# Performance work log

Hardware: AMD Instinct MI355X
Metric: run time of the kernel (lower is better)

The kernel has to match this reference:

```python
import jax, jax.numpy as jnp
import numpy as np

N_CLASS = 8192
FEAT_DIM = 1024
BATCH = 1024
PROTO_M = 0.95
TEMP = 0.1
BASE_TEMP = 0.1
EPS = 1e-12  # F.normalize eps


def setup_inputs() -> dict:
    key = jax.random.key(0)
    k1, k2, k3 = jax.random.split(key, 3)
    features = jax.random.normal(k1, (BATCH, FEAT_DIM), dtype=jnp.float32)
    labels = jax.random.randint(k2, (BATCH,), 0, N_CLASS)
    prototypes = jax.random.normal(k3, (N_CLASS, FEAT_DIM), dtype=jnp.float32)
    # init_class_prototypes ends with F.normalize(prototypes, dim=1)
    prototypes = prototypes / jnp.maximum(
        jnp.linalg.norm(prototypes, axis=1, keepdims=True), EPS)
    return {"features": features, "labels": labels, "prototypes": prototypes}


def _ema_update(prototypes, features, labels):
    # Sequential per-sample EMA scatter update (order matters for repeated labels),
    # expressed as a lax.scan over the batch.
    def step(protos, fl):
        f, l = fl
        row = protos[l] * PROTO_M + f * (1.0 - PROTO_M)
        row = row / jnp.maximum(jnp.linalg.norm(row), EPS)  # F.normalize(dim=0)
        return protos.at[l].set(row), None

    protos, _ = jax.lax.scan(step, prototypes, (features, labels))
    return protos


def reference(features, labels, prototypes):
    protos = _ema_update(prototypes, features, labels)  # [C, D]
    logits = jnp.matmul(protos, protos.T) / TEMP        # [C, C]
    exp_l = jnp.exp(logits)
    # mask = off-diagonal ones (labels are arange(n_class)), so the masked sum
    # is the row sum minus the diagonal; mask.sum(1) == n_class - 1 (never NaN).
    sum_neg = exp_l.sum(axis=1) - jnp.diagonal(exp_l)   # [C]
    mean_prob_neg = jnp.log(sum_neg / jnp.float32(N_CLASS - 1))
    loss = (TEMP / BASE_TEMP) * jnp.mean(mean_prob_neg)
    return loss
```

## Files before the change

kernel.cpp:

```cpp
#include <hip/hip_runtime.h>
#include <math.h>

#define C 8192
#define D 1024
#define BATCH 1024
#define PM 0.95f
#define PMC 0.05f
#define INVT_SCALED 0.15625f

typedef unsigned char u8;
typedef __attribute__((ext_vector_type(16))) float f32x16;

#define GLOBAL_AS(p) ((const __attribute__((address_space(1))) void*)(p))
#define LDS_AS(p) ((__attribute__((address_space(3))) void*)(p))

__global__ __launch_bounds__(256) void ema_split_kernel(const float* __restrict__ feat,
                                                        const int* __restrict__ labels,
                                                        const float* __restrict__ protos,
                                                        u8* __restrict__ P8,
                                                        float* __restrict__ rowsum,
                                                        float* __restrict__ out) {
    __shared__ int sl[BATCH];
    const int t = threadIdx.x, w = t >> 6, lane = t & 63;
    const int c = blockIdx.x * 4 + w;

    if (blockIdx.x < 32) rowsum[blockIdx.x * 256 + t] = 0.0f;
    if (blockIdx.x == 0 && t == 0) out[0] = 0.0f;

    for (int i = t; i < BATCH; i += 256) sl[i] = labels[i];
    __syncthreads();

    float4 v[4];
    #pragma unroll
    for (int s = 0; s < 4; ++s)
        v[s] = *(const float4*)(protos + (size_t)c * D + s * 256 + lane * 4);

    for (int base = 0; base < BATCH; base += 64) {
        unsigned long long mask = __ballot(sl[base + lane] == c);
        while (mask) {
            const int b = __ffsll((long long)mask) - 1;
            mask &= mask - 1;
            const int idx = base + b;
            float ss = 0.0f;
            #pragma unroll
            for (int s = 0; s < 4; ++s) {
                const float4 f = *(const float4*)(feat + (size_t)idx * D + s * 256 + lane * 4);
                v[s].x = v[s].x * PM + f.x * PMC;
                v[s].y = v[s].y * PM + f.y * PMC;
                v[s].z = v[s].z * PM + f.z * PMC;
                v[s].w = v[s].w * PM + f.w * PMC;
                ss += v[s].x * v[s].x + v[s].y * v[s].y + v[s].z * v[s].z + v[s].w * v[s].w;
            }
            #pragma unroll
            for (int off = 32; off > 0; off >>= 1) ss += __shfl_xor(ss, off);
            const float inv = 1.0f / fmaxf(sqrtf(ss), 1e-12f);
            #pragma unroll
            for (int s = 0; s < 4; ++s) {
                v[s].x *= inv; v[s].y *= inv; v[s].z *= inv; v[s].w *= inv;
            }
        }
    }

    u8* ob = P8 + (size_t)(c >> 5) * 32768 + (c & 31) * 8;
    #pragma unroll
    for (int s = 0; s < 4; ++s) {
        const int k0 = s * 256 + lane * 4;
        const size_t off = (size_t)(k0 >> 4) * 512 + ((k0 >> 3) & 1) * 256 + (k0 & 7);
        int p = __builtin_amdgcn_cvt_pk_fp8_f32(v[s].x * 8.0f, v[s].y * 8.0f, 0, false);
        p = __builtin_amdgcn_cvt_pk_fp8_f32(v[s].z * 8.0f, v[s].w * 8.0f, p, true);
        *(unsigned int*)(ob + off) = (unsigned int)p;
    }
}

__global__ __launch_bounds__(256, 4) void gram8_kernel(const u8* __restrict__ P8,
                                                       float* __restrict__ rowsum) {
    __shared__ u8 lds[5][8192];
    const int t = threadIdx.x, w = t >> 6, lane = t & 63;
    const int bb = blockIdx.x;

    const int qi = w >> 1, qj = w & 1;
    const int aoff = qi * 2048 + lane * 8;
    const int boff = 4096 + qj * 2048 + lane * 8;
    const int ldsA = w * 1024, ldsB = 4096 + w * 1024;

    const int nt = (bb % 33 == 0) ? 3 : 2;

    f32x16 acc[2][2];
    long fa[2][2], fb[2][2];

#define STAGE(KC, BUF)                                                         \
    __builtin_amdgcn_global_load_lds(GLOBAL_AS(gsrcA + (size_t)(KC) * 1024),   \
                                     LDS_AS(&lds[BUF][ldsA]), 16, 0, 0);       \
    __builtin_amdgcn_global_load_lds(GLOBAL_AS(gsrcB + (size_t)(KC) * 1024),   \
                                     LDS_AS(&lds[BUF][ldsB]), 16, 0, 0);

#define PF(SET, BUF, KK)                                                       \
    fa[SET][0] = *(const long*)&lds[BUF][aoff + (KK) * 512];                   \
    fa[SET][1] = *(const long*)&lds[BUF][aoff + 1024 + (KK) * 512];            \
    fb[SET][0] = *(const long*)&lds[BUF][boff + (KK) * 512];                   \
    fb[SET][1] = *(const long*)&lds[BUF][boff + 1024 + (KK) * 512];

#define MFMA4(SET)                                                             \
    acc[0][0] = __builtin_amdgcn_mfma_f32_32x32x16_fp8_fp8(fa[SET][0], fb[SET][0], acc[0][0], 0, 0, 0); \
    acc[0][1] = __builtin_amdgcn_mfma_f32_32x32x16_fp8_fp8(fa[SET][0], fb[SET][1], acc[0][1], 0, 0, 0); \
    acc[1][0] = __builtin_amdgcn_mfma_f32_32x32x16_fp8_fp8(fa[SET][1], fb[SET][0], acc[1][0], 0, 0, 0); \
    acc[1][1] = __builtin_amdgcn_mfma_f32_32x32x16_fp8_fp8(fa[SET][1], fb[SET][1], acc[1][1], 0, 0, 0);

#define WAITV(N) asm volatile("s_waitcnt vmcnt(" #N ")" ::: "memory")

    for (int tt = 0; tt < nt; ++tt) {
        const int l = (tt == 2) ? 2048 + bb / 33 : 2 * bb + tt;
        int rem = l, bi = 0;
        while (rem >= 64 - bi) { rem -= 64 - bi; ++bi; }
        const int bj = bi + rem;
        const bool diag = (bi == bj);

        const u8* gsrcA = P8 + (size_t)(bi * 4 + w) * 32768 + lane * 16;
        const u8* gsrcB = P8 + (size_t)(bj * 4 + w) * 32768 + lane * 16;

        #pragma unroll
        for (int a = 0; a < 2; ++a)
            #pragma unroll
            for (int b = 0; b < 2; ++b)
                #pragma unroll
                for (int e = 0; e < 16; ++e) acc[a][b][e] = 0.0f;

        __syncthreads();

        STAGE(0, 0); STAGE(1, 1); STAGE(2, 2); STAGE(3, 3);
        WAITV(4);
        __builtin_amdgcn_s_barrier();
        PF(0, 0, 0);

        int cb = 0;
        for (int kc = 0; kc < 28; ++kc) {
            const int sb = (cb >= 1) ? cb - 1 : 4;
            STAGE(kc + 4, sb);
            const int nb = (cb == 4) ? 0 : cb + 1;
            PF(1, cb, 1);
            MFMA4(0);
            PF(0, nb, 0);
            MFMA4(1);
            WAITV(4);
            __builtin_amdgcn_s_barrier();
            cb = nb;
        }
        PF(1, 3, 1); MFMA4(0);
        PF(0, 4, 0); MFMA4(1);
        WAITV(2); __builtin_amdgcn_s_barrier();
        PF(1, 4, 1); MFMA4(0);
        PF(0, 0, 0); MFMA4(1);
        WAITV(0); __builtin_amdgcn_s_barrier();
        PF(1, 0, 1); MFMA4(0);
        PF(0, 1, 0); MFMA4(1);
        PF(1, 1, 1); MFMA4(0);
        MFMA4(1);

        __syncthreads();
        float* rpart = (float*)&lds[0][0];
        float* cpart = (float*)&lds[0][512];
        if (t < 128) { rpart[t] = 0.0f; cpart[t] = 0.0f; }
        __syncthreads();
        const int half = lane >> 5, col = lane & 31;
        float csum[2] = {0.0f, 0.0f};
        #pragma unroll
        for (int ti = 0; ti < 2; ++ti) {
            float rs[16];
            #pragma unroll
            for (int reg = 0; reg < 16; ++reg) rs[reg] = 0.0f;
            #pragma unroll
            for (int tj = 0; tj < 2; ++tj) {
                const int lj = qj * 64 + tj * 32 + col;
                #pragma unroll
                for (int reg = 0; reg < 16; ++reg) {
                    const int li = qi * 64 + ti * 32 + (reg & 3) + 8 * (reg >> 2) + 4 * half;
                    float e = __expf(acc[ti][tj][reg] * INVT_SCALED);
                    if (diag && li >= lj) e = 0.0f;
                    rs[reg] += e;
                    csum[tj] += e;
                }
            }
            #pragma unroll
            for (int reg = 0; reg < 16; ++reg) {
                float v = rs[reg];
                v += __shfl_xor(v, 1); v += __shfl_xor(v, 2); v += __shfl_xor(v, 4);
                v += __shfl_xor(v, 8); v += __shfl_xor(v, 16);
                if (col == 0)
                    atomicAdd(&rpart[qi * 64 + ti * 32 + (reg & 3) + 8 * (reg >> 2) + 4 * half], v);
            }
        }
        #pragma unroll
        for (int tj = 0; tj < 2; ++tj) {
            float v = csum[tj];
            v += __shfl_xor(v, 32);
            if (half == 0) atomicAdd(&cpart[qj * 64 + tj * 32 + col], v);
        }
        __syncthreads();
        if (t < 128) atomicAdd(&rowsum[bi * 128 + t], rpart[t]);
        else         atomicAdd(&rowsum[bj * 128 + (t - 128)], cpart[t - 128]);
    }
}

__global__ __launch_bounds__(256) void final2_kernel(const float* __restrict__ rowsum,
                                                     float* __restrict__ out) {
    __shared__ float red[4];
    const int t = threadIdx.x;
    const int i = blockIdx.x * 256 + t;
    float v = logf(rowsum[i] * (1.0f / (float)(C - 1)));
    #pragma unroll
    for (int off = 32; off > 0; off >>= 1) v += __shfl_down(v, off);
    if ((t & 63) == 0) red[t >> 6] = v;
    __syncthreads();
    if (t == 0)
        atomicAdd(out, (red[0] + red[1] + red[2] + red[3]) * (1.0f / (float)C));
}

extern "C" void kernel_launch(void* const* d_in, const int* in_sizes, int n_in,
                              void* d_out, int out_size, void* d_ws, size_t ws_size,
                              hipStream_t stream) {
    const float* feat = (const float*)d_in[0];
    const int* labels = (const int*)d_in[1];
    const float* protos = (const float*)d_in[2];
    float* out = (float*)d_out;
    float* rowsum = (float*)d_ws;
    u8* P8 = (u8*)((char*)d_ws + 32768);

    ema_split_kernel<<<C / 4, 256, 0, stream>>>(feat, labels, protos, P8, rowsum, out);
    gram8_kernel<<<1024, 256, 0, stream>>>(P8, rowsum);
    final2_kernel<<<C / 256, 256, 0, stream>>>(rowsum, out);
}
```

Measured before the change: 159.8 us.

## Give each wave private LDS double buffer and drop per-step block barriers in gram kernel

Each wave now stages its own A and B row slices into a private double-buffered LDS region, so the 5-deep shared ring and its per-iteration block barriers are replaced by per-wave vmcnt/lgkmcnt waits. The tile-to-block mapping is changed to a strided strip assignment (r = bb&7) that interleaves short and long triangle strips, likely for L2 locality and load balance. The cost is that waves no longer share staged data, so each wave loads twice as much from global/L2 and the prefetch depth drops from four stages to two. That raises memory traffic and latency exposure in exchange for removing barrier stalls.

```diff
diff --git a/kernel.cpp b/kernel.cpp
--- a/kernel.cpp
+++ b/kernel.cpp
@@ -74,49 +74,60 @@
 
 __global__ __launch_bounds__(256, 4) void gram8_kernel(const u8* __restrict__ P8,
                                                        float* __restrict__ rowsum) {
-    __shared__ u8 lds[5][8192];
+    __shared__ u8 lds[4][2][4096];
     const int t = threadIdx.x, w = t >> 6, lane = t & 63;
     const int bb = blockIdx.x;
+    const int r = bb & 7;
+    const int s = bb >> 3;
 
     const int qi = w >> 1, qj = w & 1;
-    const int aoff = qi * 2048 + lane * 8;
-    const int boff = 4096 + qj * 2048 + lane * 8;
-    const int ldsA = w * 1024, ldsB = 4096 + w * 1024;
-
-    const int nt = (bb % 33 == 0) ? 3 : 2;
+
+    int nt = 2, extra = 0;
+    if (s == 0 || s == 33 || s == 66 || s == 99) { nt = 3; extra = 256 + s / 33; }
 
     f32x16 acc[2][2];
     long fa[2][2], fb[2][2];
 
-#define STAGE(KC, BUF)                                                         \
-    __builtin_amdgcn_global_load_lds(GLOBAL_AS(gsrcA + (size_t)(KC) * 1024),   \
-                                     LDS_AS(&lds[BUF][ldsA]), 16, 0, 0);       \
-    __builtin_amdgcn_global_load_lds(GLOBAL_AS(gsrcB + (size_t)(KC) * 1024),   \
-                                     LDS_AS(&lds[BUF][ldsB]), 16, 0, 0);
-
-#define PF(SET, BUF, KK)                                                       \
-    fa[SET][0] = *(const long*)&lds[BUF][aoff + (KK) * 512];                   \
-    fa[SET][1] = *(const long*)&lds[BUF][aoff + 1024 + (KK) * 512];            \
-    fb[SET][0] = *(const long*)&lds[BUF][boff + (KK) * 512];                   \
-    fb[SET][1] = *(const long*)&lds[BUF][boff + 1024 + (KK) * 512];
-
-#define MFMA4(SET)                                                             \
-    acc[0][0] = __builtin_amdgcn_mfma_f32_32x32x16_fp8_fp8(fa[SET][0], fb[SET][0], acc[0][0], 0, 0, 0); \
-    acc[0][1] = __builtin_amdgcn_mfma_f32_32x32x16_fp8_fp8(fa[SET][0], fb[SET][1], acc[0][1], 0, 0, 0); \
-    acc[1][0] = __builtin_amdgcn_mfma_f32_32x32x16_fp8_fp8(fa[SET][1], fb[SET][0], acc[1][0], 0, 0, 0); \
-    acc[1][1] = __builtin_amdgcn_mfma_f32_32x32x16_fp8_fp8(fa[SET][1], fb[SET][1], acc[1][1], 0, 0, 0);
+#define STAGE(KC, BUF)                                                             \
+    __builtin_amdgcn_global_load_lds(GLOBAL_AS(gA + (size_t)(KC) * 1024),          \
+                                     LDS_AS(&lds[w][BUF][0]), 16, 0, 0);           \
+    __builtin_amdgcn_global_load_lds(GLOBAL_AS(gA + (size_t)(KC) * 1024 + 32768),  \
+                                     LDS_AS(&lds[w][BUF][1024]), 16, 0, 0);        \
+    __builtin_amdgcn_global_load_lds(GLOBAL_AS(gB + (size_t)(KC) * 1024),          \
+                                     LDS_AS(&lds[w][BUF][2048]), 16, 0, 0);        \
+    __builtin_amdgcn_global_load_lds(GLOBAL_AS(gB + (size_t)(KC) * 1024 + 32768),  \
+                                     LDS_AS(&lds[w][BUF][3072]), 16, 0, 0);
+
+#define PF(KK, BUF)                                                                \
+    fa[KK][0] = *(const long*)&lds[w][BUF][(KK) * 512 + lane * 8];                 \
+    fa[KK][1] = *(const long*)&lds[w][BUF][1024 + (KK) * 512 + lane * 8];          \
+    fb[KK][0] = *(const long*)&lds[w][BUF][2048 + (KK) * 512 + lane * 8];          \
+    fb[KK][1] = *(const long*)&lds[w][BUF][3072 + (KK) * 512 + lane * 8];
+
+#define MFMA4(KK)                                                                  \
+    acc[0][0] = __builtin_amdgcn_mfma_f32_32x32x16_fp8_fp8(fa[KK][0], fb[KK][0], acc[0][0], 0, 0, 0); \
+    acc[0][1] = __builtin_amdgcn_mfma_f32_32x32x16_fp8_fp8(fa[KK][0], fb[KK][1], acc[0][1], 0, 0, 0); \
+    acc[1][0] = __builtin_amdgcn_mfma_f32_32x32x16_fp8_fp8(fa[KK][1], fb[KK][0], acc[1][0], 0, 0, 0); \
+    acc[1][1] = __builtin_amdgcn_mfma_f32_32x32x16_fp8_fp8(fa[KK][1], fb[KK][1], acc[1][1], 0, 0, 0);
 
 #define WAITV(N) asm volatile("s_waitcnt vmcnt(" #N ")" ::: "memory")
+#define WAITL()  asm volatile("s_waitcnt lgkmcnt(0)" ::: "memory")
 
     for (int tt = 0; tt < nt; ++tt) {
-        const int l = (tt == 2) ? 2048 + bb / 33 : 2 * bb + tt;
-        int rem = l, bi = 0;
-        while (rem >= 64 - bi) { rem -= 64 - bi; ++bi; }
-        const int bj = bi + rem;
+        const int l = (tt == 2) ? extra : 2 * s + tt;
+        int mm = l, bi = 0;
+        #pragma unroll
+        for (int s8 = 0; s8 < 8; ++s8) {
+            const int strip = (s8 & 1) ? ((s8 >> 1) * 16 + 15 - r) : ((s8 >> 1) * 16 + r);
+            const int n = 64 - strip;
+            if (mm < n) { bi = strip; break; }
+            mm -= n;
+        }
+        const int bj = bi + mm;
         const bool diag = (bi == bj);
 
-        const u8* gsrcA = P8 + (size_t)(bi * 4 + w) * 32768 + lane * 16;
-        const u8* gsrcB = P8 + (size_t)(bj * 4 + w) * 32768 + lane * 16;
+        const u8* gA = P8 + (size_t)(bi * 4 + 2 * qi) * 32768 + lane * 16;
+        const u8* gB = P8 + (size_t)(bj * 4 + 2 * qj) * 32768 + lane * 16;
 
         #pragma unroll
         for (int a = 0; a < 2; ++a)
@@ -127,38 +138,26 @@
 
         __syncthreads();
 
-        STAGE(0, 0); STAGE(1, 1); STAGE(2, 2); STAGE(3, 3);
+        STAGE(0, 0); STAGE(1, 1);
+
+        int cur = 0;
+        for (int kc = 0; kc < 30; ++kc) {
+            WAITV(4);
+            PF(0, cur); PF(1, cur);
+            MFMA4(0); MFMA4(1);
+            WAITL();
+            STAGE(kc + 2, cur);
+            cur ^= 1;
+        }
         WAITV(4);
-        __builtin_amdgcn_s_barrier();
-        PF(0, 0, 0);
-
-        int cb = 0;
-        for (int kc = 0; kc < 28; ++kc) {
-            const int sb = (cb >= 1) ? cb - 1 : 4;
-            STAGE(kc + 4, sb);
-            const int nb = (cb == 4) ? 0 : cb + 1;
-            PF(1, cb, 1);
-            MFMA4(0);
-            PF(0, nb, 0);
-            MFMA4(1);
-            WAITV(4);
-            __builtin_amdgcn_s_barrier();
-            cb = nb;
-        }
-        PF(1, 3, 1); MFMA4(0);
-        PF(0, 4, 0); MFMA4(1);
-        WAITV(2); __builtin_amdgcn_s_barrier();
-        PF(1, 4, 1); MFMA4(0);
-        PF(0, 0, 0); MFMA4(1);
-        WAITV(0); __builtin_amdgcn_s_barrier();
-        PF(1, 0, 1); MFMA4(0);
-        PF(0, 1, 0); MFMA4(1);
-        PF(1, 1, 1); MFMA4(0);
-        MFMA4(1);
-
-        __syncthreads();
-        float* rpart = (float*)&lds[0][0];
-        float* cpart = (float*)&lds[0][512];
+        PF(0, cur); PF(1, cur); MFMA4(0); MFMA4(1);
+        cur ^= 1;
+        WAITV(0);
+        PF(0, cur); PF(1, cur); MFMA4(0); MFMA4(1);
+
+        __syncthreads();
+        float* rpart = (float*)&lds[0][0][0];
+        float* cpart = (float*)&lds[0][0][512];
         if (t < 128) { rpart[t] = 0.0f; cpart[t] = 0.0f; }
         __syncthreads();
         const int half = lane >> 5, col = lane & 31;
```

New measurement: 168.8 us. 1.06x slower.
